# Kernel optimization log

Measured on AMD Instinct MI355X. Metric: run time of the kernel, lower is better.

Reference implementation:

```python
import jax, jax.numpy as jnp
import numpy as np
from jax import lax

N_CFG = [[4, 4]]
D_CFG = [4, 8, 8]
B, H, W_IMG = 64, 32, 32


def _make_idx(N=N_CFG, D=D_CFG):
    """Replicates CNNModel.createConnectivity and converts each layer's sparse
    connectivity rows into a dense [node, fan_in] gather-index array (all rows in a
    layer have equal fan-in for these factorizations)."""
    N_ = int(np.prod(N[0]))
    I = np.eye(N_)
    Wm = []
    for n in N:
        v = 1
        for n_ in n:
            w = np.zeros((N_, N_))
            for k in range(n_):
                w = w + np.roll(I, axis=0, shift=k * v)
            Wm.append(w)
            v = v * n_
    conn = [np.kron(np.ones((D[i + 1], D[i])), Wm[i]) for i in range(len(Wm))]
    nodes = [int(d) * N_ for d in D]
    conn.insert(0, np.ones((nodes[0], 3)))
    idx = []
    for c in conn:
        rows = [np.nonzero(c[k])[0] for k in range(c.shape[0])]
        idx.append(jnp.asarray(np.stack(rows), dtype=jnp.int32))
    return idx, nodes

IDX, NODES = _make_idx()  # fan-ins: 3, 16, 32; nodes: 64, 128, 128


def setup_inputs() -> dict:
    key = jax.random.key(0)
    ks = jax.random.split(key, 11)
    nrm = lambda k, s: (jax.random.normal(k, s, jnp.float32) * 0.05)
    return {
        "inputs": jax.random.normal(ks[0], (B, H, W_IMG, 3), jnp.float32),
        "cw0": nrm(ks[1], (3, 3, 3, NODES[0])),
        "cb0": nrm(ks[2], (NODES[0],)),
        "cw1": nrm(ks[3], (3, 3, 16, NODES[1])),
        "cb1": nrm(ks[4], (NODES[1],)),
        "cw2": nrm(ks[5], (3, 3, 32, NODES[2])),
        "cb2": nrm(ks[6], (NODES[2],)),
        "dw1": nrm(ks[7], (H * W_IMG * NODES[2], 50)),
        "db1": nrm(ks[8], (50,)),
        "dw2": nrm(ks[9], (50, 10)),
        "db2": nrm(ks[10], (10,)),
    }


def _sparse_layer(x, idx, w, b):
    # x: [B,H,W,C_prev]; idx: [node, F]; w: [3,3,F,node]; b: [node]
    # Gather each node's fan-in channels, then run all per-node 1-filter 3x3 convs
    # as a single grouped convolution (feature_group_count = node).
    node, F = idx.shape
    g = x[..., idx.reshape(-1)]  # [B,H,W,node*F]
    y = lax.conv_general_dilated(
        g, w, window_strides=(1, 1), padding="SAME",
        dimension_numbers=("NHWC", "HWIO", "NHWC"),
        feature_group_count=node)  # [B,H,W,node]
    return jax.nn.relu(y + b)


def reference(inputs, cw0, cb0, cw1, cb1, cw2, cb2, dw1, db1, dw2, db2):
    x = inputs.reshape(-1, H, W_IMG, 3)
    x = _sparse_layer(x, IDX[0], cw0, cb0)
    x = _sparse_layer(x, IDX[1], cw1, cb1)
    x = _sparse_layer(x, IDX[2], cw2, cb2)
    x = x.reshape(x.shape[0], -1)  # Flatten (NHWC row-major, matches TF)
    x = jax.nn.relu(x @ dw1 + db1)
    return jax.nn.softmax(x @ dw2 + db2, axis=-1)
```

## Files before the change

kernel.cpp:

```cpp
#include <hip/hip_runtime.h>
#include <math.h>

typedef unsigned short u16;
typedef unsigned int u32;
typedef __attribute__((ext_vector_type(8))) short short8v;
typedef __attribute__((ext_vector_type(4))) float f32x4;

#define X0PN_OFF 4734976
#define X2B_OFF  7102464
#define W1Q_OFF  11300000
#define W2P_OFF  11330000

__device__ __forceinline__ u16 f2bf(float f) {
    union { float f; u32 i; } c; c.f = f;
    u32 r = c.i + 0x7fffu + ((c.i >> 16) & 1u);
    return (u16)(r >> 16);
}
__device__ __forceinline__ int Sf(int i0, int m) {
    return (i0 >= 3) ? (i0 - 3 + m) : ((m <= i0) ? m : (12 + m));
}

__global__ __launch_bounds__(256) void prep_l0(const float* __restrict__ cw1,
    const float* __restrict__ cw2, const float* __restrict__ in,
    const float* __restrict__ cw0, const float* __restrict__ cb0,
    u16* __restrict__ x0pn, u16* __restrict__ x1pn,
    u16* __restrict__ w1q, u16* __restrict__ w2p) {
    int bi = blockIdx.x;
    if (bi < 1080) {
        int t = bi * 256 + threadIdx.x;
        if (t < 202752) {
            uint4 z = {0u, 0u, 0u, 0u};
            int cell, v; u16* base; int nch;
            if (t < 67584) { v = t & 7; cell = t >> 3; base = x0pn; nch = 64; }
            else { int u = t - 67584; v = u & 15; cell = u >> 4; base = x1pn; nch = 128; }
            int b = cell / 132, ci = cell - b * 132;
            int y, x;
            if (ci < 34)       { y = 0;       x = ci; }
            else if (ci < 68)  { y = 33;      x = ci - 34; }
            else if (ci < 100) { y = ci - 67; x = 0; }
            else               { y = ci - 99; x = 33; }
            *(uint4*)(base + ((b * 34 + y) * 34 + x) * nch + v * 8) = z;
            return;
        }
        int u0 = t - 202752;
        if (u0 < 36864) {
            int j = u0 & 7, lane = (u0 >> 3) & 63;
            int tp = u0 >> 9;
            int tap = tp % 9, pr = tp / 9;
            int n = lane & 15;
            int k = 8 * (lane >> 4) + j;
            float v = 0.f;
            if (n < 8) {
                if (k < 16) {
                    int f = 4 * (k & 3) + (k >> 2);
                    v = cw1[(tap * 16 + f) * 128 + 2 * pr + 16 * n];
                }
            } else {
                if (k >= 16) {
                    int k2 = k - 16;
                    int f = 4 * (k2 & 3) + (k2 >> 2);
                    v = cw1[(tap * 16 + f) * 128 + 2 * pr + 1 + 16 * (n - 8)];
                }
            }
            w1q[u0] = f2bf(v);
        } else {
            int u = u0 - 36864;
            int j = u & 7, lane = (u >> 3) & 63;
            int nt = (u >> 9) & 1;
            int gt = u >> 10, tap = gt % 9, g = gt / 9;
            int k = 8 * (lane >> 4) + j;
            int f = 4 * (k >> 2) + (k & 3);
            int n = g + 4 * (nt * 16 + (lane & 15));
            w2p[u] = f2bf(cw2[(tap * 32 + f) * 128 + n]);
        }
        return;
    }
    int lb = bi - 1080;
    int b = lb >> 3, sub = lb & 7;
    int t = threadIdx.x, lane = t & 63, wv = t >> 6;
    int col = lane & 15, khi = lane >> 4;

    short8v Bf[4];
#pragma unroll
    for (int nb = 0; nb < 4; ++nb) {
        union { short8v v; u16 e[8]; } B;
#pragma unroll
        for (int j = 0; j < 8; ++j) {
            int k = 8 * khi + j;
            B.e[j] = (k < 27) ? f2bf(cw0[k * 64 + nb * 16 + col]) : (u16)0;
        }
        Bf[nb] = B.v;
    }
    float bias[4];
#pragma unroll
    for (int nb = 0; nb < 4; ++nb) bias[nb] = cb0[nb * 16 + col];

    for (int it = 0; it < 2; ++it) {
        int tile = sub * 8 + wv * 2 + it;
        int py = tile >> 1, px0 = (tile & 1) * 16;
        union { short8v v; u16 e[8]; } A;
#pragma unroll
        for (int j = 0; j < 8; ++j) {
            int k = 8 * khi + j;
            float v = 0.f;
            if (k < 27) {
                int tap = k / 3, c = k - 3 * tap;
                int dy = tap / 3, dx = tap - 3 * dy;
                int y = py + dy - 1, x = px0 + col + dx - 1;
                if ((unsigned)y < 32u && (unsigned)x < 32u)
                    v = in[((b * 32 + y) * 32 + x) * 3 + c];
            }
            A.e[j] = f2bf(v);
        }
        f32x4 acc[4];
#pragma unroll
        for (int nb = 0; nb < 4; ++nb) {
            f32x4 ci = {bias[nb], bias[nb], bias[nb], bias[nb]};
            acc[nb] = __builtin_amdgcn_mfma_f32_16x16x32_bf16(A.v, Bf[nb], ci, 0, 0, 0);
        }
#pragma unroll
        for (int r = 0; r < 4; ++r) {
            int px_l = 4 * khi + r;
            u32 lo = (u32)f2bf(fmaxf(acc[0][r], 0.f)) | ((u32)f2bf(fmaxf(acc[1][r], 0.f)) << 16);
            u32 hi = (u32)f2bf(fmaxf(acc[2][r], 0.f)) | ((u32)f2bf(fmaxf(acc[3][r], 0.f)) << 16);
            uint2 pk = {lo, hi};
            *(uint2*)(x0pn + ((size_t)(b * 34 + py + 1) * 34 + px0 + px_l + 1) * 64 + 4 * col) = pk;
        }
    }
}

__global__ __launch_bounds__(256) void l1_mfma(const u16* __restrict__ x0pn,
    const u16* __restrict__ w1q, const float* __restrict__ cb1, u16* __restrict__ x1pn) {
    __shared__ __align__(16) unsigned char x0s[26112];
    int bi = blockIdx.x;
    int xcd = bi & 7, slot = bi >> 3;
    int b = xcd * 8 + (slot >> 4);
    int rem = slot & 15;
    int rq = rem >> 1, pp = rem & 1;
    int t = threadIdx.x, lane = t & 63, wv = t >> 6;

    {
        const u16* src = x0pn + (size_t)(b * 1156 + rq * 136) * 64;
        for (int c = t; c < 1632; c += 256) {
            uint4 v = *(const uint4*)(src + c * 8);
            int p = c >> 3;
            int dst = (c * 16) ^ ((p & 7) << 4);
            *(uint4*)(x0s + dst) = v;
        }
    }
    __syncthreads();

    int col = lane & 15, khi = lane >> 4;

    int pr = pp * 4 + wv;
    int i0a = 2 * pr, i0b = 2 * pr + 1;
    int i0g = (khi >= 2) ? i0b : i0a;
    int mb = 2 * (khi & 1);
    int o0 = 8 * Sf(i0g, mb), o1 = 8 * Sf(i0g, mb + 1);

    short8v wf[9];
#pragma unroll
    for (int tap = 0; tap < 9; ++tap)
        wf[tap] = *(const short8v*)(w1q + ((pr * 9 + tap) * 64 + lane) * 8);

    int node = (col < 8) ? (i0a + 16 * col) : (i0b + 16 * (col - 8));
    float bv = cb1[node];
    int cperm = 32 * (node & 3) + (node >> 2);

    for (int mt = 0; mt < 8; ++mt) {
        int row_l = mt >> 1, cbase = (mt & 1) * 16;
        f32x4 acc = {bv, bv, bv, bv};
        int pbase = row_l * 34 + cbase + col;
#pragma unroll
        for (int tap = 0; tap < 9; ++tap) {
            const int dy = tap / 3, dx = tap % 3;
            int p = pbase + dy * 34 + dx;
            int sw = (p & 7) << 4;
            int base = p * 128;
            union { short8v v; uint2 h[2]; } A;
            A.h[0] = *(const uint2*)(x0s + base + (o0 ^ sw));
            A.h[1] = *(const uint2*)(x0s + base + (o1 ^ sw));
            acc = __builtin_amdgcn_mfma_f32_16x16x32_bf16(A.v, wf[tap], acc, 0, 0, 0);
        }
        int prow = rq * 4 + row_l + 1;
        u16* ob = x1pn + ((size_t)(b * 34 + prow) * 34) * 128 + cperm;
#pragma unroll
        for (int r = 0; r < 4; ++r) {
            int pcol = cbase + khi * 4 + r + 1;
            ob[pcol * 128] = f2bf(fmaxf(acc[r], 0.f));
        }
    }
}

__global__ __launch_bounds__(256) void l2_mfma(const u16* __restrict__ x1pn,
    const u16* __restrict__ w2p, const float* __restrict__ cb2, u16* __restrict__ x2b) {
    __shared__ __align__(16) u16 x1s[6 * 34 * 32];
    int bi = blockIdx.x;
    int xcd = bi & 7, slot = bi >> 3;
    int b = xcd * 8 + (slot >> 5);
    int rem = slot & 31;
    int rq = rem >> 2, g = rem & 3;
    int t = threadIdx.x, lane = t & 63, wvi = t >> 6;
    int col = lane & 15, khi = lane >> 4;

    {
        const u16* src = x1pn + (size_t)(b * 34 + rq * 4) * (34 * 128) + g * 32;
        for (int c = t; c < 816; c += 256) {
            int row = c / 136, e = c - row * 136;
            int px = e >> 2, part = e & 3;
            uint4 v = *(const uint4*)(src + (size_t)row * (34 * 128) + px * 128 + part * 8);
            *(uint4*)(x1s + (row * 34 + px) * 32 + part * 8) = v;
        }
    }
    __syncthreads();

    short8v wf[9][2];
#pragma unroll
    for (int tap = 0; tap < 9; ++tap)
#pragma unroll
        for (int nt = 0; nt < 2; ++nt)
            wf[tap][nt] = *(const short8v*)(w2p + (((g * 9 + tap) * 2 + nt) * 64 + lane) * 8);

    float bv0 = cb2[g + 4 * col];
    float bv1 = cb2[g + 4 * (16 + col)];

    int y = rq * 4 + wvi;
    f32x4 acc[2][2];
    acc[0][0] = (f32x4){bv0, bv0, bv0, bv0}; acc[0][1] = (f32x4){bv1, bv1, bv1, bv1};
    acc[1][0] = acc[0][0];                   acc[1][1] = acc[0][1];
#pragma unroll
    for (int tap = 0; tap < 9; ++tap) {
        const int dy = tap / 3, dx = tap % 3;
#pragma unroll
        for (int ms = 0; ms < 2; ++ms) {
            int px = (wvi + dy) * 34 + ms * 16 + col + dx;
            short8v a = *(const short8v*)(x1s + px * 32 + khi * 8);
            acc[ms][0] = __builtin_amdgcn_mfma_f32_16x16x32_bf16(a, wf[tap][0], acc[ms][0], 0, 0, 0);
            acc[ms][1] = __builtin_amdgcn_mfma_f32_16x16x32_bf16(a, wf[tap][1], acc[ms][1], 0, 0, 0);
        }
    }
#pragma unroll
    for (int ms = 0; ms < 2; ++ms)
#pragma unroll
        for (int nt = 0; nt < 2; ++nt) {
#pragma unroll
            for (int r = 0; r < 4; ++r) {
                int px = ms * 16 + 4 * khi + r;
                x2b[(size_t)b * 131072 + ((g * 2 + nt) * 1024 + y * 32 + px) * 16 + col]
                    = f2bf(fmaxf(acc[ms][nt][r], 0.f));
            }
        }
}

#define D1_NB 512
__global__ __launch_bounds__(256) void d1_mfma(const u16* __restrict__ x2b,
                                               const float* __restrict__ dw1,
                                               float* __restrict__ partial) {
    int kb = blockIdx.x;
    int t = threadIdx.x, lane = t & 63, w = t >> 6;
    int col = lane & 15, khi = lane >> 4;
    int n = 16 * w + col;
    f32x4 acc[4];
#pragma unroll
    for (int m = 0; m < 4; ++m) acc[m] = (f32x4){0.f, 0.f, 0.f, 0.f};

    int k0 = kb * 256;
#pragma unroll 2
    for (int ks = 0; ks < 8; ++ks) {
        int kbase = k0 + ks * 32 + 8 * khi;
        int c0 = kbase & 15;
        int q = kbase >> 4;
        int g = q >> 11, nt = (q >> 10) & 1, pix = q & 1023;
        union { short8v v; u16 e[8]; } Bf;
        if (n < 50) {
            const float* wp = dw1 + (size_t)(pix * 128 + g + 64 * nt + 4 * c0) * 50 + n;
#pragma unroll
            for (int j = 0; j < 8; ++j) Bf.e[j] = f2bf(wp[j * 200]);
        } else {
            Bf.v = (short8v)0;
        }
#pragma unroll
        for (int m = 0; m < 4; ++m) {
            short8v A = *(const short8v*)(x2b + (size_t)(m * 16 + col) * 131072 + kbase);
            acc[m] = __builtin_amdgcn_mfma_f32_16x16x32_bf16(A, Bf.v, acc[m], 0, 0, 0);
        }
    }
#pragma unroll
    for (int m = 0; m < 4; ++m)
#pragma unroll
        for (int r = 0; r < 4; ++r) {
            int brow = m * 16 + khi * 4 + r;
            partial[((size_t)brow * D1_NB + kb) * 64 + n] = acc[m][r];
        }
}

__global__ __launch_bounds__(256) void rd2_kernel(const float* __restrict__ partial,
    const float* __restrict__ db1, const float* __restrict__ dw2,
    const float* __restrict__ db2, float* __restrict__ out) {
    __shared__ float sm[4][64];
    __shared__ float hs[64];
    __shared__ float as[10];
    int b = blockIdx.x;
    int t = threadIdx.x;
    int j = t & 63, pp = t >> 6;
    const float* pb = partial + ((size_t)b * D1_NB + pp * 128) * 64 + j;
    float s0 = 0.f, s1 = 0.f, s2 = 0.f, s3 = 0.f;
    for (int cb = 0; cb < 128; cb += 4) {
        s0 += pb[(cb + 0) * 64];
        s1 += pb[(cb + 1) * 64];
        s2 += pb[(cb + 2) * 64];
        s3 += pb[(cb + 3) * 64];
    }
    sm[pp][j] = (s0 + s1) + (s2 + s3);
    __syncthreads();
    if (pp == 0) {
        float h = (sm[0][j] + sm[1][j]) + (sm[2][j] + sm[3][j]);
        hs[j] = (j < 50) ? fmaxf(h + db1[j], 0.f) : 0.f;
    }
    __syncthreads();
    if (t < 10) {
        float a = db2[t];
        for (int i = 0; i < 50; ++i) a += hs[i] * dw2[i * 10 + t];
        as[t] = a;
    }
    __syncthreads();
    if (t == 0) {
        float mx = as[0];
#pragma unroll
        for (int q = 1; q < 10; ++q) mx = fmaxf(mx, as[q]);
        float e[10], s = 0.f;
#pragma unroll
        for (int q = 0; q < 10; ++q) { e[q] = expf(as[q] - mx); s += e[q]; }
        float inv = 1.f / s;
#pragma unroll
        for (int q = 0; q < 10; ++q) out[b * 10 + q] = e[q] * inv;
    }
}

extern "C" void kernel_launch(void* const* d_in, const int* in_sizes, int n_in,
                              void* d_out, int out_size, void* d_ws, size_t ws_size,
                              hipStream_t stream) {
    const float* inputs = (const float*)d_in[0];
    const float* cw0 = (const float*)d_in[1];
    const float* cb0 = (const float*)d_in[2];
    const float* cw1 = (const float*)d_in[3];
    const float* cb1 = (const float*)d_in[4];
    const float* cw2 = (const float*)d_in[5];
    const float* cb2 = (const float*)d_in[6];
    const float* dw1 = (const float*)d_in[7];
    const float* db1 = (const float*)d_in[8];
    const float* dw2 = (const float*)d_in[9];
    const float* db2 = (const float*)d_in[10];
    float* out = (float*)d_out;

    float* ws = (float*)d_ws;
    u16* x1pn = (u16*)ws;
    u16* x0pn = (u16*)(ws + X0PN_OFF);
    u16* x2b  = (u16*)(ws + X2B_OFF);
    float* partial = ws;
    u16* w1q  = (u16*)(ws + W1Q_OFF);
    u16* w2p  = (u16*)(ws + W2P_OFF);

    prep_l0<<<1592, 256, 0, stream>>>(cw1, cw2, inputs, cw0, cb0, x0pn, x1pn, w1q, w2p);
    l1_mfma<<<1024, 256, 0, stream>>>(x0pn, w1q, cb1, x1pn);
    l2_mfma<<<2048, 256, 0, stream>>>(x1pn, w2p, cb2, x2b);
    d1_mfma<<<D1_NB, 256, 0, stream>>>(x2b, dw1, partial);
    rd2_kernel<<<64, 256, 0, stream>>>(partial, db1, dw2, db2, out);
}
```

Baseline: 62.54 us.

## Restructure layer-1 weights, coalesce x2b layout, widen final reduction

Layer 1 now uses a new packed weight layout where each wave handles one group and two node blocks, issuing two MFMAs per tap with contiguous 16-byte LDS loads instead of split 8-byte gathers. The grid is halved and x1 writes go to a contiguous channel layout. The x2b intermediate is reordered so that each dense-layer K block reads a contiguous 256-element slab per batch row. The final reduction kernel uses 1024 threads with 16 partial sums to shorten the serial loop. In exchange, layer 1 does twice the MFMA work, since many weight entries are zero-padded.

```diff
diff --git a/kernel.cpp b/kernel.cpp
--- a/kernel.cpp
+++ b/kernel.cpp
@@ -9,24 +9,21 @@
 #define X0PN_OFF 4734976
 #define X2B_OFF  7102464
 #define W1Q_OFF  11300000
-#define W2P_OFF  11330000
+#define W2P_OFF  11340000
 
 __device__ __forceinline__ u16 f2bf(float f) {
     union { float f; u32 i; } c; c.f = f;
     u32 r = c.i + 0x7fffu + ((c.i >> 16) & 1u);
     return (u16)(r >> 16);
 }
-__device__ __forceinline__ int Sf(int i0, int m) {
-    return (i0 >= 3) ? (i0 - 3 + m) : ((m <= i0) ? m : (12 + m));
-}
 
 __global__ __launch_bounds__(256) void prep_l0(const float* __restrict__ cw1,
     const float* __restrict__ cw2, const float* __restrict__ in,
     const float* __restrict__ cw0, const float* __restrict__ cb0,
     u16* __restrict__ x0pn, u16* __restrict__ x1pn,
-    u16* __restrict__ w1q, u16* __restrict__ w2p) {
+    u16* __restrict__ w1q2, u16* __restrict__ w2p) {
     int bi = blockIdx.x;
-    if (bi < 1080) {
+    if (bi < 1224) {
         int t = bi * 256 + threadIdx.x;
         if (t < 202752) {
             uint4 z = {0u, 0u, 0u, 0u};
@@ -42,29 +39,30 @@
             *(uint4*)(base + ((b * 34 + y) * 34 + x) * nch + v * 8) = z;
             return;
         }
-        int u0 = t - 202752;
-        if (u0 < 36864) {
+        if (t < 276480) {
+            int u0 = t - 202752;
             int j = u0 & 7, lane = (u0 >> 3) & 63;
-            int tp = u0 >> 9;
-            int tap = tp % 9, pr = tp / 9;
-            int n = lane & 15;
-            int k = 8 * (lane >> 4) + j;
+            int idx = u0 >> 9;
+            int h = idx & 1;
+            int tapi = (idx >> 1) % 9;
+            int gj = (idx >> 1) / 9;
+            int g = gj >> 1, jb = gj & 1;
+            int colB = lane & 15, khi = lane >> 4;
+            int kk = 8 * khi + j;
+            int r = 8 * h + (kk >> 2);
+            int ci = kk & 3;
+            int n = 64 * jb + 4 * colB + g;
+            int i0 = 4 * (colB & 3) + g;
+            int m = -1;
+            if (i0 >= 3) { if (r >= i0 - 3 && r <= i0) m = r - i0 + 3; }
+            else { if (r <= i0) m = r; else if (r >= 13 + i0) m = r - 12; }
             float v = 0.f;
-            if (n < 8) {
-                if (k < 16) {
-                    int f = 4 * (k & 3) + (k >> 2);
-                    v = cw1[(tap * 16 + f) * 128 + 2 * pr + 16 * n];
-                }
-            } else {
-                if (k >= 16) {
-                    int k2 = k - 16;
-                    int f = 4 * (k2 & 3) + (k2 >> 2);
-                    v = cw1[(tap * 16 + f) * 128 + 2 * pr + 1 + 16 * (n - 8)];
-                }
-            }
-            w1q[u0] = f2bf(v);
-        } else {
-            int u = u0 - 36864;
+            if (m >= 0) v = cw1[(tapi * 16 + 4 * ci + m) * 128 + n];
+            w1q2[u0] = f2bf(v);
+            return;
+        }
+        {
+            int u = t - 276480;
             int j = u & 7, lane = (u >> 3) & 63;
             int nt = (u >> 9) & 1;
             int gt = u >> 10, tap = gt % 9, g = gt / 9;
@@ -75,7 +73,7 @@
         }
         return;
     }
-    int lb = bi - 1080;
+    int lb = bi - 1224;
     int b = lb >> 3, sub = lb & 7;
     int t = threadIdx.x, lane = t & 63, wv = t >> 6;
     int col = lane & 15, khi = lane >> 4;
@@ -130,14 +128,13 @@
 }
 
 __global__ __launch_bounds__(256) void l1_mfma(const u16* __restrict__ x0pn,
-    const u16* __restrict__ w1q, const float* __restrict__ cb1, u16* __restrict__ x1pn) {
+    const u16* __restrict__ w1q2, const float* __restrict__ cb1, u16* __restrict__ x1pn) {
     __shared__ __align__(16) unsigned char x0s[26112];
     int bi = blockIdx.x;
     int xcd = bi & 7, slot = bi >> 3;
-    int b = xcd * 8 + (slot >> 4);
-    int rem = slot & 15;
-    int rq = rem >> 1, pp = rem & 1;
-    int t = threadIdx.x, lane = t & 63, wv = t >> 6;
+    int b = xcd * 8 + (slot >> 3), rq = slot & 7;
+    int t = threadIdx.x, lane = t & 63;
+    int g = t >> 6;
 
     {
         const u16* src = x0pn + (size_t)(b * 1156 + rq * 136) * 64;
@@ -152,42 +149,39 @@
 
     int col = lane & 15, khi = lane >> 4;
 
-    int pr = pp * 4 + wv;
-    int i0a = 2 * pr, i0b = 2 * pr + 1;
-    int i0g = (khi >= 2) ? i0b : i0a;
-    int mb = 2 * (khi & 1);
-    int o0 = 8 * Sf(i0g, mb), o1 = 8 * Sf(i0g, mb + 1);
-
-    short8v wf[9];
-#pragma unroll
-    for (int tap = 0; tap < 9; ++tap)
-        wf[tap] = *(const short8v*)(w1q + ((pr * 9 + tap) * 64 + lane) * 8);
-
-    int node = (col < 8) ? (i0a + 16 * col) : (i0b + 16 * (col - 8));
-    float bv = cb1[node];
-    int cperm = 32 * (node & 3) + (node >> 2);
-
-    for (int mt = 0; mt < 8; ++mt) {
-        int row_l = mt >> 1, cbase = (mt & 1) * 16;
-        f32x4 acc = {bv, bv, bv, bv};
-        int pbase = row_l * 34 + cbase + col;
-#pragma unroll
-        for (int tap = 0; tap < 9; ++tap) {
-            const int dy = tap / 3, dx = tap % 3;
-            int p = pbase + dy * 34 + dx;
-            int sw = (p & 7) << 4;
-            int base = p * 128;
-            union { short8v v; uint2 h[2]; } A;
-            A.h[0] = *(const uint2*)(x0s + base + (o0 ^ sw));
-            A.h[1] = *(const uint2*)(x0s + base + (o1 ^ sw));
-            acc = __builtin_amdgcn_mfma_f32_16x16x32_bf16(A.v, wf[tap], acc, 0, 0, 0);
-        }
-        int prow = rq * 4 + row_l + 1;
-        u16* ob = x1pn + ((size_t)(b * 34 + prow) * 34) * 128 + cperm;
-#pragma unroll
-        for (int r = 0; r < 4; ++r) {
-            int pcol = cbase + khi * 4 + r + 1;
-            ob[pcol * 128] = f2bf(fmaxf(acc[r], 0.f));
+    for (int jb = 0; jb < 2; ++jb) {
+        short8v wf[9][2];
+#pragma unroll
+        for (int tap = 0; tap < 9; ++tap)
+#pragma unroll
+            for (int h = 0; h < 2; ++h)
+                wf[tap][h] = *(const short8v*)(w1q2 + (size_t)((((g * 2 + jb) * 9 + tap) * 2 + h) * 64 + lane) * 8);
+
+        float bv = cb1[64 * jb + 4 * col + g];
+
+        for (int mt = 0; mt < 8; ++mt) {
+            int row_l = mt >> 1, cbase = (mt & 1) * 16;
+            f32x4 acc = {bv, bv, bv, bv};
+            int pbase = row_l * 34 + cbase + col;
+#pragma unroll
+            for (int tap = 0; tap < 9; ++tap) {
+                const int dy = tap / 3, dx = tap % 3;
+                int p = pbase + dy * 34 + dx;
+                int sw = (p & 7) << 4;
+                int base = p * 128;
+#pragma unroll
+                for (int h = 0; h < 2; ++h) {
+                    short8v A = *(const short8v*)(x0s + base + ((64 * h + 16 * khi) ^ sw));
+                    acc = __builtin_amdgcn_mfma_f32_16x16x32_bf16(A, wf[tap][h], acc, 0, 0, 0);
+                }
+            }
+            int prow = rq * 4 + row_l + 1;
+            u16* ob = x1pn + ((size_t)(b * 34 + prow) * 34) * 128 + 32 * g + 16 * jb + col;
+#pragma unroll
+            for (int r = 0; r < 4; ++r) {
+                int pcol = cbase + 4 * khi + r + 1;
+                ob[pcol * 128] = f2bf(fmaxf(acc[r], 0.f));
+            }
         }
     }
 }
@@ -243,11 +237,10 @@
     for (int ms = 0; ms < 2; ++ms)
 #pragma unroll
         for (int nt = 0; nt < 2; ++nt) {
+            size_t kbase = ((size_t)((g * 2 + nt) * 64 + y * 2 + ms) * 64 + b) * 256;
 #pragma unroll
             for (int r = 0; r < 4; ++r) {
-                int px = ms * 16 + 4 * khi + r;
-                x2b[(size_t)b * 131072 + ((g * 2 + nt) * 1024 + y * 32 + px) * 16 + col]
-                    = f2bf(fmaxf(acc[ms][nt][r], 0.f));
+                x2b[kbase + (4 * khi + r) * 16 + col] = f2bf(fmaxf(acc[ms][nt][r], 0.f));
             }
         }
 }
@@ -264,10 +257,9 @@
 #pragma unroll
     for (int m = 0; m < 4; ++m) acc[m] = (f32x4){0.f, 0.f, 0.f, 0.f};
 
-    int k0 = kb * 256;
 #pragma unroll 2
     for (int ks = 0; ks < 8; ++ks) {
-        int kbase = k0 + ks * 32 + 8 * khi;
+        int kbase = kb * 256 + ks * 32 + 8 * khi;
         int c0 = kbase & 15;
         int q = kbase >> 4;
         int g = q >> 11, nt = (q >> 10) & 1, pix = q & 1023;
@@ -281,7 +273,8 @@
         }
 #pragma unroll
         for (int m = 0; m < 4; ++m) {
-            short8v A = *(const short8v*)(x2b + (size_t)(m * 16 + col) * 131072 + kbase);
+            short8v A = *(const short8v*)(x2b + ((size_t)kb * 64 + m * 16 + col) * 256
+                                          + ks * 32 + 8 * khi);
             acc[m] = __builtin_amdgcn_mfma_f32_16x16x32_bf16(A, Bf.v, acc[m], 0, 0, 0);
         }
     }
@@ -294,18 +287,18 @@
         }
 }
 
-__global__ __launch_bounds__(256) void rd2_kernel(const float* __restrict__ partial,
+__global__ __launch_bounds__(1024) void rd2_kernel(const float* __restrict__ partial,
     const float* __restrict__ db1, const float* __restrict__ dw2,
     const float* __restrict__ db2, float* __restrict__ out) {
-    __shared__ float sm[4][64];
+    __shared__ float sm[16][64];
     __shared__ float hs[64];
     __shared__ float as[10];
     int b = blockIdx.x;
     int t = threadIdx.x;
     int j = t & 63, pp = t >> 6;
-    const float* pb = partial + ((size_t)b * D1_NB + pp * 128) * 64 + j;
+    const float* pb = partial + ((size_t)b * D1_NB + pp * 32) * 64 + j;
     float s0 = 0.f, s1 = 0.f, s2 = 0.f, s3 = 0.f;
-    for (int cb = 0; cb < 128; cb += 4) {
+    for (int cb = 0; cb < 32; cb += 4) {
         s0 += pb[(cb + 0) * 64];
         s1 += pb[(cb + 1) * 64];
         s2 += pb[(cb + 2) * 64];
@@ -314,7 +307,9 @@
     sm[pp][j] = (s0 + s1) + (s2 + s3);
     __syncthreads();
     if (pp == 0) {
-        float h = (sm[0][j] + sm[1][j]) + (sm[2][j] + sm[3][j]);
+        float h = 0.f;
+#pragma unroll
+        for (int q = 0; q < 16; ++q) h += sm[q][j];
         hs[j] = (j < 50) ? fmaxf(h + db1[j], 0.f) : 0.f;
     }
     __syncthreads();
@@ -358,12 +353,12 @@
     u16* x0pn = (u16*)(ws + X0PN_OFF);
     u16* x2b  = (u16*)(ws + X2B_OFF);
     float* partial = ws;
-    u16* w1q  = (u16*)(ws + W1Q_OFF);
+    u16* w1q2 = (u16*)(ws + W1Q_OFF);
     u16* w2p  = (u16*)(ws + W2P_OFF);
 
-    prep_l0<<<1592, 256, 0, stream>>>(cw1, cw2, inputs, cw0, cb0, x0pn, x1pn, w1q, w2p);
-    l1_mfma<<<1024, 256, 0, stream>>>(x0pn, w1q, cb1, x1pn);
+    prep_l0<<<1736, 256, 0, stream>>>(cw1, cw2, inputs, cw0, cb0, x0pn, x1pn, w1q2, w2p);
+    l1_mfma<<<512, 256, 0, stream>>>(x0pn, w1q2, cb1, x1pn);
     l2_mfma<<<2048, 256, 0, stream>>>(x1pn, w2p, cb2, x2b);
     d1_mfma<<<D1_NB, 256, 0, stream>>>(x2b, dw1, partial);
-    rd2_kernel<<<64, 256, 0, stream>>>(partial, db1, dw2, db2, out);
-}
+    rd2_kernel<<<64, 1024, 0, stream>>>(partial, db1, dw2, db2, out);
+}
```

After: 75.81 us. +21.2%, slower.
